# Optimization experiments

Measured on AMD Instinct MI355X. Metric: run time of the kernel, lower is better.

Reference implementation:

```python
import jax, jax.numpy as jnp
import numpy as np

EPS = 1e-8  # torch F.cosine_similarity eps


def setup_inputs() -> dict:
    key = jax.random.key(0)
    k1, k2, k3 = jax.random.split(key, 3)
    bn, cn, dim = 4096, 8192, 1024
    x = jax.random.normal(k1, (bn, dim), dtype=jnp.float32)
    positive = jax.random.normal(k2, (bn, dim), dtype=jnp.float32)
    negative = jax.random.normal(k3, (cn, dim), dtype=jnp.float32)
    return {"x": x, "positive": positive, "negative": negative}


def reference(x, positive, negative):
    bn = x.shape[0]
    nx = jnp.linalg.norm(x, axis=1)          # (bn,)
    npos = jnp.linalg.norm(positive, axis=1)  # (bn,)
    nneg = jnp.linalg.norm(negative, axis=1)  # (cn,)
    # positive cosine similarity, torch-style eps clamp on norm product
    sim = jnp.sum(x * positive, axis=1) / jnp.maximum(nx * npos, EPS)  # (bn,)
    # negative cosine similarities via one matmul instead of (bn,cn,dim) repeats
    neg_sim = (x @ negative.T) / jnp.maximum(nx[:, None] * nneg[None, :], EPS)  # (bn,cn)
    p = jnp.exp(sim) / jnp.sum(jnp.exp(neg_sim), axis=1)  # (bn,)
    loss = -jnp.sum(jnp.log(p)) / bn
    return loss
```

## Files before the change

### kernel.cpp

```cpp
#include <hip/hip_runtime.h>
#include <stdint.h>
#include <stddef.h>

#define DIM 1024
#define EPS 1e-8f

typedef __attribute__((ext_vector_type(4))) float f32x4;

__device__ __forceinline__ void async_copy16(const void* g, void* l) {
    __builtin_amdgcn_global_load_lds(
        (__attribute__((address_space(1))) void*)const_cast<void*>(g),
        (__attribute__((address_space(3))) void*)(l), 16, 0, 0);
}

#define PIPE_SYNC(N) asm volatile("s_waitcnt vmcnt(" #N ")\n\ts_barrier" ::: "memory")

__global__ __launch_bounds__(256)
void prep_all(const float* __restrict__ x, const float* __restrict__ pos,
              const float* __restrict__ neg,
              unsigned char* __restrict__ Xn, unsigned char* __restrict__ Nn,
              float* __restrict__ simOut, float* __restrict__ rowsum, int bn) {
    const int lane = threadIdx.x & 63;
    const int wave = threadIdx.x >> 6;
    const int grow = blockIdx.x * 4 + wave;
    const bool isX = grow < bn;
    const int row  = isX ? grow : grow - bn;
    const float* src = isX ? x : neg;
    unsigned char* dst = isX ? Xn : Nn;

    const float4* s = (const float4*)(src + (size_t)row * DIM);
    float4 xv[4], pv[4];
    float sxx = 0.f, spp = 0.f, sxp = 0.f;
#pragma unroll
    for (int i = 0; i < 4; i++) {
        xv[i] = s[lane + 64 * i];
        sxx += xv[i].x * xv[i].x + xv[i].y * xv[i].y + xv[i].z * xv[i].z + xv[i].w * xv[i].w;
    }
    if (isX) {
        const float4* p = (const float4*)(pos + (size_t)row * DIM);
#pragma unroll
        for (int i = 0; i < 4; i++) {
            pv[i] = p[lane + 64 * i];
            spp += pv[i].x * pv[i].x + pv[i].y * pv[i].y + pv[i].z * pv[i].z + pv[i].w * pv[i].w;
            sxp += xv[i].x * pv[i].x + xv[i].y * pv[i].y + xv[i].z * pv[i].z + xv[i].w * pv[i].w;
        }
#pragma unroll
        for (int off = 1; off < 64; off <<= 1) {
            sxx += __shfl_xor(sxx, off);
            spp += __shfl_xor(spp, off);
            sxp += __shfl_xor(sxp, off);
        }
    } else {
#pragma unroll
        for (int off = 1; off < 64; off <<= 1) sxx += __shfl_xor(sxx, off);
    }
    const float nx  = sqrtf(sxx);
    const float inv = (nx > 0.f) ? (16.f / nx) : 0.f;
    if (isX && lane == 0) {
        const float np = sqrtf(spp);
        simOut[row] = sxp / fmaxf(nx * np, EPS);
        rowsum[row] = 0.f;
    }
    uint4 w;
    unsigned int t;
    t = __builtin_amdgcn_cvt_pk_fp8_f32(xv[0].x * inv, xv[0].y * inv, 0, false);
    w.x = __builtin_amdgcn_cvt_pk_fp8_f32(xv[0].z * inv, xv[0].w * inv, t, true);
    t = __builtin_amdgcn_cvt_pk_fp8_f32(xv[1].x * inv, xv[1].y * inv, 0, false);
    w.y = __builtin_amdgcn_cvt_pk_fp8_f32(xv[1].z * inv, xv[1].w * inv, t, true);
    t = __builtin_amdgcn_cvt_pk_fp8_f32(xv[2].x * inv, xv[2].y * inv, 0, false);
    w.z = __builtin_amdgcn_cvt_pk_fp8_f32(xv[2].z * inv, xv[2].w * inv, t, true);
    t = __builtin_amdgcn_cvt_pk_fp8_f32(xv[3].x * inv, xv[3].y * inv, 0, false);
    w.w = __builtin_amdgcn_cvt_pk_fp8_f32(xv[3].z * inv, xv[3].w * inv, t, true);
    ((uint4*)(dst + (size_t)row * DIM))[lane] = w;
}

__global__ __launch_bounds__(256)
void gemm_exp_rowsum(const unsigned char* __restrict__ Xn,
                     const unsigned char* __restrict__ Nn,
                     float* __restrict__ rowsum) {
    constexpr int KB   = DIM;
    constexpr int BK   = 64;
    constexpr int BUFB = 128 * BK;
    __shared__ __align__(16) unsigned char Ash[3][BUFB];
    __shared__ __align__(16) unsigned char Bsh[3][BUFB];

    const int tid  = threadIdx.x;
    const int lane = tid & 63;
    const int wave = tid >> 6;
    const int rowBase = blockIdx.y * 128;
    const int colBase = blockIdx.x * 128;

    const int srow   = lane >> 2;
    const int schunk = (lane & 3) ^ ((srow >> 1) & 3);
    const unsigned char* gA = Xn + (size_t)(rowBase + wave * 16 + srow) * KB + schunk * 16;
    const unsigned char* gB = Nn + (size_t)(colBase + wave * 16 + srow) * KB + schunk * 16;
    const int lgrp0 = (wave * 16) * BK;
    const int lgrp1 = (wave * 16 + 64) * BK;

    const f32x4 fz = {0.f, 0.f, 0.f, 0.f};
    f32x4 acc[4][4];
#pragma unroll
    for (int mi = 0; mi < 4; mi++)
#pragma unroll
        for (int ni = 0; ni < 4; ni++) acc[mi][ni] = fz;

    const int m0   = (wave >> 1) * 64;
    const int n0   = (wave & 1) * 64;
    const int quad = lane >> 4;
    const int mrow = lane & 15;
    const int kx   = (mrow >> 1) & 3;
    const int cb0  = (((quad >> 1) ^ kx) << 4) + (quad & 1) * 8;

    int aoff[4], boff[4];
#pragma unroll
    for (int i = 0; i < 4; i++) {
        aoff[i] = (m0 + i * 16 + mrow) * BK + cb0;
        boff[i] = (n0 + i * 16 + mrow) * BK + cb0;
    }

#define STAGE(buf, stg)                                                  \
    do {                                                                 \
        const int kq = (stg) * BK;                                       \
        async_copy16(gA + kq,            &Ash[buf][lgrp0]);              \
        async_copy16(gA + 64 * KB + kq,  &Ash[buf][lgrp1]);              \
        async_copy16(gB + kq,            &Bsh[buf][lgrp0]);              \
        async_copy16(gB + 64 * KB + kq,  &Bsh[buf][lgrp1]);              \
    } while (0)

#define COMPUTE(buf)                                                     \
    do {                                                                 \
        _Pragma("unroll")                                                \
        for (int ks2 = 0; ks2 < 2; ks2++) {                              \
            const int cx = ks2 * 32;              \
            long af[4], bf[4];                                           \
            _Pragma("unroll")                                            \
            for (int i = 0; i < 4; i++) {                                \
                af[i] = *(const long*)&Ash[buf][aoff[i] ^ cx];           \
                bf[i] = *(const long*)&Bsh[buf][boff[i] ^ cx];           \
            }                                                            \
            _Pragma("unroll")                                            \
            for (int mi = 0; mi < 4; mi++)                               \
                _Pragma("unroll")                                        \
                for (int ni = 0; ni < 4; ni++)                           \
                    acc[mi][ni] = __builtin_amdgcn_mfma_f32_16x16x32_fp8_fp8( \
                        af[mi], bf[ni], acc[mi][ni], 0, 0, 0);           \
        }                                                                \
    } while (0)

    STAGE(0, 0);
    STAGE(1, 1);
    for (int it = 0; it < 4; it++) {
        const int s = 3 * it + 2;
        PIPE_SYNC(4); STAGE(2, s);     COMPUTE(0);
        PIPE_SYNC(4); STAGE(0, s + 1); COMPUTE(1);
        PIPE_SYNC(4); STAGE(1, s + 2); COMPUTE(2);
    }
    PIPE_SYNC(4); STAGE(2, 14); COMPUTE(0);
    PIPE_SYNC(4); STAGE(0, 15); COMPUTE(1);
    PIPE_SYNC(4);               COMPUTE(2);
    PIPE_SYNC(0);               COMPUTE(0);
#undef STAGE
#undef COMPUTE

#pragma unroll
    for (int mi = 0; mi < 4; mi++) {
        float rs0 = 0.f, rs1 = 0.f, rs2 = 0.f, rs3 = 0.f;
#pragma unroll
        for (int ni = 0; ni < 4; ni++) {
            rs0 += __expf(acc[mi][ni].x * 0.00390625f);
            rs1 += __expf(acc[mi][ni].y * 0.00390625f);
            rs2 += __expf(acc[mi][ni].z * 0.00390625f);
            rs3 += __expf(acc[mi][ni].w * 0.00390625f);
        }
#pragma unroll
        for (int off = 1; off < 16; off <<= 1) {
            rs0 += __shfl_xor(rs0, off);
            rs1 += __shfl_xor(rs1, off);
            rs2 += __shfl_xor(rs2, off);
            rs3 += __shfl_xor(rs3, off);
        }
        if ((lane & 15) == 0) {
            const int r = rowBase + m0 + mi * 16 + quad * 4;
            atomicAdd(&rowsum[r + 0], rs0);
            atomicAdd(&rowsum[r + 1], rs1);
            atomicAdd(&rowsum[r + 2], rs2);
            atomicAdd(&rowsum[r + 3], rs3);
        }
    }
}

__global__ __launch_bounds__(1024)
void loss_kernel(const float* __restrict__ rowsum, const float* __restrict__ sim,
                 float* __restrict__ out, int bn) {
    const int tid  = threadIdx.x;
    const int lane = tid & 63;
    const int wave = tid >> 6;
    float acc = 0.f;
    for (int i = tid; i < bn; i += 1024) acc += logf(rowsum[i]) - sim[i];
#pragma unroll
    for (int off = 1; off < 64; off <<= 1) acc += __shfl_xor(acc, off);
    __shared__ float red[16];
    if (lane == 0) red[wave] = acc;
    __syncthreads();
    if (tid == 0) {
        float t = 0.f;
#pragma unroll
        for (int i = 0; i < 16; i++) t += red[i];
        out[0] = t / (float)bn;
    }
}

extern "C" void kernel_launch(void* const* d_in, const int* in_sizes, int n_in,
                              void* d_out, int out_size, void* d_ws, size_t ws_size,
                              hipStream_t stream) {
    const float* x   = (const float*)d_in[0];
    const float* pos = (const float*)d_in[1];
    const float* neg = (const float*)d_in[2];
    const int bn = in_sizes[0] / DIM;
    const int cn = in_sizes[2] / DIM;

    unsigned char* Xn = (unsigned char*)d_ws;
    unsigned char* Nn = Xn + (size_t)bn * DIM;
    float* sim    = (float*)(Nn + (size_t)cn * DIM);
    float* rowsum = sim + bn;

    prep_all<<<dim3((bn + cn) / 4), dim3(256), 0, stream>>>(x, pos, neg, Xn, Nn, sim, rowsum, bn);
    gemm_exp_rowsum<<<dim3(cn / 128, bn / 128), dim3(256), 0, stream>>>(Xn, Nn, rowsum);
    loss_kernel<<<dim3(1), dim3(1024), 0, stream>>>(rowsum, sim, (float*)d_out, bn);
}
```

Baseline: 180.1 us.

## Permute fp8 K layout in prep so GEMM reads 16-byte LDS fragments

New measurement: 166.8 us. 1.08x faster.

```diff
diff --git a/kernel.cpp b/kernel.cpp
--- a/kernel.cpp
+++ b/kernel.cpp
@@ -6,6 +6,7 @@
 #define EPS 1e-8f
 
 typedef __attribute__((ext_vector_type(4))) float f32x4;
+typedef __attribute__((ext_vector_type(2))) long longx2;
 
 __device__ __forceinline__ void async_copy16(const void* g, void* l) {
     __builtin_amdgcn_global_load_lds(
@@ -61,17 +62,21 @@
         simOut[row] = sxp / fmaxf(nx * np, EPS);
         rowsum[row] = 0.f;
     }
-    uint4 w;
     unsigned int t;
     t = __builtin_amdgcn_cvt_pk_fp8_f32(xv[0].x * inv, xv[0].y * inv, 0, false);
-    w.x = __builtin_amdgcn_cvt_pk_fp8_f32(xv[0].z * inv, xv[0].w * inv, t, true);
+    unsigned int q0 = __builtin_amdgcn_cvt_pk_fp8_f32(xv[0].z * inv, xv[0].w * inv, t, true);
     t = __builtin_amdgcn_cvt_pk_fp8_f32(xv[1].x * inv, xv[1].y * inv, 0, false);
-    w.y = __builtin_amdgcn_cvt_pk_fp8_f32(xv[1].z * inv, xv[1].w * inv, t, true);
+    unsigned int q1 = __builtin_amdgcn_cvt_pk_fp8_f32(xv[1].z * inv, xv[1].w * inv, t, true);
     t = __builtin_amdgcn_cvt_pk_fp8_f32(xv[2].x * inv, xv[2].y * inv, 0, false);
-    w.z = __builtin_amdgcn_cvt_pk_fp8_f32(xv[2].z * inv, xv[2].w * inv, t, true);
+    unsigned int q2 = __builtin_amdgcn_cvt_pk_fp8_f32(xv[2].z * inv, xv[2].w * inv, t, true);
     t = __builtin_amdgcn_cvt_pk_fp8_f32(xv[3].x * inv, xv[3].y * inv, 0, false);
-    w.w = __builtin_amdgcn_cvt_pk_fp8_f32(xv[3].z * inv, xv[3].w * inv, t, true);
-    ((uint4*)(dst + (size_t)row * DIM))[lane] = w;
+    unsigned int q3 = __builtin_amdgcn_cvt_pk_fp8_f32(xv[3].z * inv, xv[3].w * inv, t, true);
+
+    const int m  = lane & 3;
+    const int d0 = (m & 1) * 32 + (m >> 1) * 8;
+    unsigned char* wbase = dst + (size_t)row * DIM + (lane >> 2) * 64;
+    *(unsigned long long*)(wbase + d0)      = ((unsigned long long)q1 << 32) | q0;
+    *(unsigned long long*)(wbase + d0 + 16) = ((unsigned long long)q3 << 32) | q2;
 }
 
 __global__ __launch_bounds__(256)
@@ -109,13 +114,12 @@
     const int quad = lane >> 4;
     const int mrow = lane & 15;
     const int kx   = (mrow >> 1) & 3;
-    const int cb0  = (((quad >> 1) ^ kx) << 4) + (quad & 1) * 8;
 
     int aoff[4], boff[4];
 #pragma unroll
     for (int i = 0; i < 4; i++) {
-        aoff[i] = (m0 + i * 16 + mrow) * BK + cb0;
-        boff[i] = (n0 + i * 16 + mrow) * BK + cb0;
+        aoff[i] = (m0 + i * 16 + mrow) * BK + ((quad ^ kx) << 4);
+        boff[i] = (n0 + i * 16 + mrow) * BK + ((quad ^ kx) << 4);
     }
 
 #define STAGE(buf, stg)                                                  \
@@ -129,22 +133,21 @@
 
 #define COMPUTE(buf)                                                     \
     do {                                                                 \
+        longx2 a2[4], b2[4];                                             \
         _Pragma("unroll")                                                \
-        for (int ks2 = 0; ks2 < 2; ks2++) {                              \
-            const int cx = ks2 * 32;              \
-            long af[4], bf[4];                                           \
+        for (int i = 0; i < 4; i++) {                                    \
+            a2[i] = *(const longx2*)&Ash[buf][aoff[i]];                  \
+            b2[i] = *(const longx2*)&Bsh[buf][boff[i]];                  \
+        }                                                                \
+        _Pragma("unroll")                                                \
+        for (int mi = 0; mi < 4; mi++)                                   \
             _Pragma("unroll")                                            \
-            for (int i = 0; i < 4; i++) {                                \
-                af[i] = *(const long*)&Ash[buf][aoff[i] ^ cx];           \
-                bf[i] = *(const long*)&Bsh[buf][boff[i] ^ cx];           \
+            for (int ni = 0; ni < 4; ni++) {                             \
+                acc[mi][ni] = __builtin_amdgcn_mfma_f32_16x16x32_fp8_fp8( \
+                    a2[mi].x, b2[ni].x, acc[mi][ni], 0, 0, 0);           \
+                acc[mi][ni] = __builtin_amdgcn_mfma_f32_16x16x32_fp8_fp8( \
+                    a2[mi].y, b2[ni].y, acc[mi][ni], 0, 0, 0);           \
             }                                                            \
-            _Pragma("unroll")                                            \
-            for (int mi = 0; mi < 4; mi++)                               \
-                _Pragma("unroll")                                        \
-                for (int ni = 0; ni < 4; ni++)                           \
-                    acc[mi][ni] = __builtin_amdgcn_mfma_f32_16x16x32_fp8_fp8( \
-                        af[mi], bf[ni], acc[mi][ni], 0, 0, 0);           \
-        }                                                                \
     } while (0)
 
     STAGE(0, 0);
```

## Switch FP8 GEMM to 32x32x64 scaled MFMA with contiguous per-lane K layout

Applied to the files above, without the earlier changes.

Measured after the change: 280.1 us. 55.5% more time.

```diff
diff --git a/kernel.cpp b/kernel.cpp
--- a/kernel.cpp
+++ b/kernel.cpp
@@ -5,7 +5,9 @@
 #define DIM 1024
 #define EPS 1e-8f
 
-typedef __attribute__((ext_vector_type(4))) float f32x4;
+typedef int   v8i    __attribute__((ext_vector_type(8)));
+typedef int   i32x4  __attribute__((ext_vector_type(4)));
+typedef float f32x16 __attribute__((ext_vector_type(16)));
 
 __device__ __forceinline__ void async_copy16(const void* g, void* l) {
     __builtin_amdgcn_global_load_lds(
@@ -33,14 +35,14 @@
     float sxx = 0.f, spp = 0.f, sxp = 0.f;
 #pragma unroll
     for (int i = 0; i < 4; i++) {
-        xv[i] = s[lane + 64 * i];
+        xv[i] = s[lane * 4 + i];
         sxx += xv[i].x * xv[i].x + xv[i].y * xv[i].y + xv[i].z * xv[i].z + xv[i].w * xv[i].w;
     }
     if (isX) {
         const float4* p = (const float4*)(pos + (size_t)row * DIM);
 #pragma unroll
         for (int i = 0; i < 4; i++) {
-            pv[i] = p[lane + 64 * i];
+            pv[i] = p[lane * 4 + i];
             spp += pv[i].x * pv[i].x + pv[i].y * pv[i].y + pv[i].z * pv[i].z + pv[i].w * pv[i].w;
             sxp += xv[i].x * pv[i].x + xv[i].y * pv[i].y + xv[i].z * pv[i].z + xv[i].w * pv[i].w;
         }
@@ -63,13 +65,13 @@
     }
     uint4 w;
     unsigned int t;
-    t = __builtin_amdgcn_cvt_pk_fp8_f32(xv[0].x * inv, xv[0].y * inv, 0, false);
+    t   = __builtin_amdgcn_cvt_pk_fp8_f32(xv[0].x * inv, xv[0].y * inv, 0, false);
     w.x = __builtin_amdgcn_cvt_pk_fp8_f32(xv[0].z * inv, xv[0].w * inv, t, true);
-    t = __builtin_amdgcn_cvt_pk_fp8_f32(xv[1].x * inv, xv[1].y * inv, 0, false);
+    t   = __builtin_amdgcn_cvt_pk_fp8_f32(xv[1].x * inv, xv[1].y * inv, 0, false);
     w.y = __builtin_amdgcn_cvt_pk_fp8_f32(xv[1].z * inv, xv[1].w * inv, t, true);
-    t = __builtin_amdgcn_cvt_pk_fp8_f32(xv[2].x * inv, xv[2].y * inv, 0, false);
+    t   = __builtin_amdgcn_cvt_pk_fp8_f32(xv[2].x * inv, xv[2].y * inv, 0, false);
     w.z = __builtin_amdgcn_cvt_pk_fp8_f32(xv[2].z * inv, xv[2].w * inv, t, true);
-    t = __builtin_amdgcn_cvt_pk_fp8_f32(xv[3].x * inv, xv[3].y * inv, 0, false);
+    t   = __builtin_amdgcn_cvt_pk_fp8_f32(xv[3].x * inv, xv[3].y * inv, 0, false);
     w.w = __builtin_amdgcn_cvt_pk_fp8_f32(xv[3].z * inv, xv[3].w * inv, t, true);
     ((uint4*)(dst + (size_t)row * DIM))[lane] = w;
 }
@@ -97,25 +99,26 @@
     const int lgrp0 = (wave * 16) * BK;
     const int lgrp1 = (wave * 16 + 64) * BK;
 
-    const f32x4 fz = {0.f, 0.f, 0.f, 0.f};
-    f32x4 acc[4][4];
-#pragma unroll
-    for (int mi = 0; mi < 4; mi++)
-#pragma unroll
-        for (int ni = 0; ni < 4; ni++) acc[mi][ni] = fz;
+    f32x16 acc[2][2];
+#pragma unroll
+    for (int mi = 0; mi < 2; mi++)
+#pragma unroll
+        for (int ni = 0; ni < 2; ni++)
+#pragma unroll
+            for (int r = 0; r < 16; r++) acc[mi][ni][r] = 0.f;
 
     const int m0   = (wave >> 1) * 64;
     const int n0   = (wave & 1) * 64;
-    const int quad = lane >> 4;
-    const int mrow = lane & 15;
-    const int kx   = (mrow >> 1) & 3;
-    const int cb0  = (((quad >> 1) ^ kx) << 4) + (quad & 1) * 8;
-
-    int aoff[4], boff[4];
-#pragma unroll
-    for (int i = 0; i < 4; i++) {
-        aoff[i] = (m0 + i * 16 + mrow) * BK + cb0;
-        boff[i] = (n0 + i * 16 + mrow) * BK + cb0;
+    const int mrow = lane & 31;
+    const int half = lane >> 5;
+    const int key  = (mrow >> 1) & 3;
+    const int cphy = ((half << 1) ^ key) << 4;
+
+    int aoff[2], boff[2];
+#pragma unroll
+    for (int i = 0; i < 2; i++) {
+        aoff[i] = (m0 + i * 32 + mrow) * BK + cphy;
+        boff[i] = (n0 + i * 32 + mrow) * BK + cphy;
     }
 
 #define STAGE(buf, stg)                                                  \
@@ -129,22 +132,21 @@
 
 #define COMPUTE(buf)                                                     \
     do {                                                                 \
+        v8i a2[2], b2[2];                                                \
         _Pragma("unroll")                                                \
-        for (int ks2 = 0; ks2 < 2; ks2++) {                              \
-            const int cx = ks2 * 32;              \
-            long af[4], bf[4];                                           \
+        for (int i = 0; i < 2; i++) {                                    \
+            *(i32x4*)&a2[i]       = *(const i32x4*)&Ash[buf][aoff[i]];   \
+            *((i32x4*)&a2[i] + 1) = *(const i32x4*)&Ash[buf][aoff[i] ^ 16]; \
+            *(i32x4*)&b2[i]       = *(const i32x4*)&Bsh[buf][boff[i]];   \
+            *((i32x4*)&b2[i] + 1) = *(const i32x4*)&Bsh[buf][boff[i] ^ 16]; \
+        }                                                                \
+        _Pragma("unroll")                                                \
+        for (int mi = 0; mi < 2; mi++)                                   \
             _Pragma("unroll")                                            \
-            for (int i = 0; i < 4; i++) {                                \
-                af[i] = *(const long*)&Ash[buf][aoff[i] ^ cx];           \
-                bf[i] = *(const long*)&Bsh[buf][boff[i] ^ cx];           \
-            }                                                            \
-            _Pragma("unroll")                                            \
-            for (int mi = 0; mi < 4; mi++)                               \
-                _Pragma("unroll")                                        \
-                for (int ni = 0; ni < 4; ni++)                           \
-                    acc[mi][ni] = __builtin_amdgcn_mfma_f32_16x16x32_fp8_fp8( \
-                        af[mi], bf[ni], acc[mi][ni], 0, 0, 0);           \
-        }                                                                \
+            for (int ni = 0; ni < 2; ni++)                               \
+                acc[mi][ni] = __builtin_amdgcn_mfma_scale_f32_32x32x64_f8f6f4( \
+                    a2[mi], b2[ni], acc[mi][ni], 0, 0,                   \
+                    0, 0x7F7F7F7F, 0, 0x7F7F7F7F);                       \
     } while (0)
 
     STAGE(0, 0);
@@ -163,30 +165,18 @@
 #undef COMPUTE
 
 #pragma unroll
-    for (int mi = 0; mi < 4; mi++) {
-        float rs0 = 0.f, rs1 = 0.f, rs2 = 0.f, rs3 = 0.f;
-#pragma unroll
-        for (int ni = 0; ni < 4; ni++) {
-            rs0 += __expf(acc[mi][ni].x * 0.00390625f);
-            rs1 += __expf(acc[mi][ni].y * 0.00390625f);
-            rs2 += __expf(acc[mi][ni].z * 0.00390625f);
-            rs3 += __expf(acc[mi][ni].w * 0.00390625f);
+    for (int mi = 0; mi < 2; mi++)
+#pragma unroll
+        for (int r = 0; r < 16; r++) {
+            float v = __expf(acc[mi][0][r] * 0.00390625f)
+                    + __expf(acc[mi][1][r] * 0.00390625f);
+#pragma unroll
+            for (int off = 1; off < 32; off <<= 1) v += __shfl_xor(v, off);
+            if (mrow == 0) {
+                const int rloc = (r & 3) + 8 * (r >> 2) + 4 * half;
+                atomicAdd(&rowsum[rowBase + m0 + mi * 32 + rloc], v);
+            }
         }
-#pragma unroll
-        for (int off = 1; off < 16; off <<= 1) {
-            rs0 += __shfl_xor(rs0, off);
-            rs1 += __shfl_xor(rs1, off);
-            rs2 += __shfl_xor(rs2, off);
-            rs3 += __shfl_xor(rs3, off);
-        }
-        if ((lane & 15) == 0) {
-            const int r = rowBase + m0 + mi * 16 + quad * 4;
-            atomicAdd(&rowsum[r + 0], rs0);
-            atomicAdd(&rowsum[r + 1], rs1);
-            atomicAdd(&rowsum[r + 2], rs2);
-            atomicAdd(&rowsum[r + 3], rs3);
-        }
-    }
 }
 
 __global__ __launch_bounds__(1024)
@@ -224,7 +214,8 @@
     float* sim    = (float*)(Nn + (size_t)cn * DIM);
     float* rowsum = sim + bn;
 
-    prep_all<<<dim3((bn + cn) / 4), dim3(256), 0, stream>>>(x, pos, neg, Xn, Nn, sim, rowsum, bn);
+    prep_all<<<dim3((bn + cn) / 4), dim3(256), 0, stream>>>(
+        x, pos, neg, Xn, Nn, sim, rowsum, bn);
     gemm_exp_rowsum<<<dim3(cn / 128, bn / 128), dim3(256), 0, stream>>>(Xn, Nn, rowsum);
     loss_kernel<<<dim3(1), dim3(1024), 0, stream>>>(rowsum, sim, (float*)d_out, bn);
 }
```
